# Optimization experiments

Measured on AMD Instinct MI355X. Metric: run time of the kernel, lower is better.

Reference implementation:

```python
import jax, jax.numpy as jnp
import numpy as np
from jax import lax

T, D, NH, CATS = 1024, 2048, 2048, 1000


def setup_inputs() -> dict:
    key = jax.random.key(0)
    ks = jax.random.split(key, 16)
    s = 0.02
    return {
        "x": jax.random.normal(ks[0], (T, D), dtype=jnp.float32),
        "Wh": jax.random.normal(ks[1], (NH, D), dtype=jnp.float32) * s,
        "Wz": jax.random.normal(ks[2], (NH, D), dtype=jnp.float32) * s,
        "Wr": jax.random.normal(ks[3], (NH, D), dtype=jnp.float32) * s,
        "Uh": jax.random.normal(ks[4], (NH, NH), dtype=jnp.float32) * s,
        "Uz": jax.random.normal(ks[5], (NH, NH), dtype=jnp.float32) * s,
        "bz": jax.random.normal(ks[6], (NH,), dtype=jnp.float32) * s,
        "Ur": jax.random.normal(ks[7], (NH, NH), dtype=jnp.float32) * s,
        "br": jax.random.normal(ks[8], (NH,), dtype=jnp.float32) * s,
        "Wout": jax.random.normal(ks[9], (CATS, NH), dtype=jnp.float32) * s,
        "h0": jax.random.normal(ks[10], (NH,), dtype=jnp.float32),
        "zt0": jax.random.normal(ks[11], (NH,), dtype=jnp.float32),
        "htilde0": jax.random.normal(ks[12], (NH,), dtype=jnp.float32),
        "hprev0": jax.random.normal(ks[13], (NH,), dtype=jnp.float32),
    }


def reference(x, Wh, Wz, Wr, Uh, Uz, bz, Ur, br, Wout, h0, zt0, htilde0, hprev0):
    # Batch the input projections over all timesteps: [T,d] @ [d,nh] -> [T,nh]
    xh = x @ Wh.T
    xz = x @ Wz.T
    xr = x @ Wr.T

    # Faithful to the original update ORDER: h is computed from the *stale*
    # zt/htilde (from the previous iteration), then gates are refreshed.
    # The original's hadamard(a, b) = linear(a, diag(b)) is exactly a * b.
    def step(carry, xs):
        h, zt, htilde, hprev = carry
        xh_t, xz_t, xr_t = xs
        h_new = (1.0 - zt) * hprev + zt * htilde
        zt_new = jax.nn.sigmoid(xz_t + hprev @ Uz.T + bz)
        htilde_new = jnp.tanh(xh_t + hprev @ Uh.T)
        # rt = sigmoid(xr_t + hprev @ Ur.T + br)  # computed in original, never used
        return (h_new, zt_new, htilde_new, h_new), None

    (h_fin, _, _, _), _ = lax.scan(step, (h0, zt0, htilde0, hprev0), (xh, xz, xr))
    logits = h_fin @ Wout.T  # [cats]
    return jax.nn.softmax(logits, axis=0)
```

## Files before the change

### kernel.cpp

```cpp
#include <hip/hip_runtime.h>
#include <math.h>

#define TT  1024
#define DD  2048
#define NHH 2048
#define CC  1000

#define SLOT_U64 4096

__global__ __launch_bounds__(256) void k_gemm(const float* __restrict__ X,
                                              const float* __restrict__ Wh,
                                              const float* __restrict__ Wz,
                                              const float* __restrict__ bz,
                                              float* __restrict__ XH,
                                              float* __restrict__ XZ) {
    __shared__ float As[32][68];
    __shared__ float Bs[32][68];
    const int z = blockIdx.z;
    const float* __restrict__ W = z ? Wz : Wh;
    float* __restrict__ OUT = z ? XZ : XH;
    const int n0 = blockIdx.x * 64;
    const int m0 = blockIdx.y * 64;
    const int tid = threadIdx.x;
    const int tx = tid & 15, ty = tid >> 4;
    const int lr = tid >> 2;
    const int lc = (tid & 3) * 8;

    float acc[4][4] = {};
    for (int k0 = 0; k0 < DD; k0 += 32) {
        float4 a0 = *(const float4*)&X[(size_t)(m0 + lr) * DD + k0 + lc];
        float4 a1 = *(const float4*)&X[(size_t)(m0 + lr) * DD + k0 + lc + 4];
        float4 b0 = *(const float4*)&W[(size_t)(n0 + lr) * DD + k0 + lc];
        float4 b1 = *(const float4*)&W[(size_t)(n0 + lr) * DD + k0 + lc + 4];
        As[lc+0][lr]=a0.x; As[lc+1][lr]=a0.y; As[lc+2][lr]=a0.z; As[lc+3][lr]=a0.w;
        As[lc+4][lr]=a1.x; As[lc+5][lr]=a1.y; As[lc+6][lr]=a1.z; As[lc+7][lr]=a1.w;
        Bs[lc+0][lr]=b0.x; Bs[lc+1][lr]=b0.y; Bs[lc+2][lr]=b0.z; Bs[lc+3][lr]=b0.w;
        Bs[lc+4][lr]=b1.x; Bs[lc+5][lr]=b1.y; Bs[lc+6][lr]=b1.z; Bs[lc+7][lr]=b1.w;
        __syncthreads();
#pragma unroll
        for (int kk = 0; kk < 32; ++kk) {
            float4 av = *(const float4*)&As[kk][ty * 4];
            float4 bv = *(const float4*)&Bs[kk][tx * 4];
            acc[0][0] = fmaf(av.x, bv.x, acc[0][0]); acc[0][1] = fmaf(av.x, bv.y, acc[0][1]);
            acc[0][2] = fmaf(av.x, bv.z, acc[0][2]); acc[0][3] = fmaf(av.x, bv.w, acc[0][3]);
            acc[1][0] = fmaf(av.y, bv.x, acc[1][0]); acc[1][1] = fmaf(av.y, bv.y, acc[1][1]);
            acc[1][2] = fmaf(av.y, bv.z, acc[1][2]); acc[1][3] = fmaf(av.y, bv.w, acc[1][3]);
            acc[2][0] = fmaf(av.z, bv.x, acc[2][0]); acc[2][1] = fmaf(av.z, bv.y, acc[2][1]);
            acc[2][2] = fmaf(av.z, bv.z, acc[2][2]); acc[2][3] = fmaf(av.z, bv.w, acc[2][3]);
            acc[3][0] = fmaf(av.w, bv.x, acc[3][0]); acc[3][1] = fmaf(av.w, bv.y, acc[3][1]);
            acc[3][2] = fmaf(av.w, bv.z, acc[3][2]); acc[3][3] = fmaf(av.w, bv.w, acc[3][3]);
        }
        __syncthreads();
    }
    float4 bias = make_float4(0.f, 0.f, 0.f, 0.f);
    if (z) bias = *(const float4*)&bz[n0 + tx * 4];
#pragma unroll
    for (int i = 0; i < 4; ++i) {
        float4 o = make_float4(acc[i][0] + bias.x, acc[i][1] + bias.y,
                               acc[i][2] + bias.z, acc[i][3] + bias.w);
        *(float4*)&OUT[(size_t)(m0 + ty * 4 + i) * NHH + n0 + tx * 4] = o;
    }
}

__global__ __launch_bounds__(256, 1) void k_recur(
    const float* __restrict__ XH, const float* __restrict__ XZ,
    const float* __restrict__ Uh, const float* __restrict__ Uz,
    const float* __restrict__ zt0, const float* __restrict__ ht0,
    const float* __restrict__ hp0,
    unsigned long long* __restrict__ Hbuf) {
    __shared__ float Hs[2][NHH];
    const int tid  = threadIdx.x;
    const int wave = tid >> 6, lane = tid & 63;
    const int wg   = blockIdx.x;
    const int base8 = wg * 8;
    const int e0 = base8 + 2 * wave;

    float u[4][32];
#pragma unroll
    for (int r = 0; r < 2; ++r) {
        const float* __restrict__ rowz = Uz + (size_t)(e0 + r) * NHH;
        const float* __restrict__ rowh = Uh + (size_t)(e0 + r) * NHH;
#pragma unroll
        for (int c = 0; c < 8; ++c) {
            float4 vz = *(const float4*)&rowz[c * 256 + lane * 4];
            float4 vh = *(const float4*)&rowh[c * 256 + lane * 4];
            u[r][c*4+0]=vz.x; u[r][c*4+1]=vz.y; u[r][c*4+2]=vz.z; u[r][c*4+3]=vz.w;
            u[2+r][c*4+0]=vh.x; u[2+r][c*4+1]=vh.y; u[2+r][c*4+2]=vh.z; u[2+r][c*4+3]=vh.w;
        }
    }

#pragma unroll
    for (int k = 0; k < 8; ++k) Hs[0][k * 256 + tid] = hp0[k * 256 + tid];

    float p_cur = 0.f;
    if (lane < 2) {
        const int e = e0 + lane;
        float z0 = zt0[e], g0 = ht0[e], p0 = hp0[e];
        p_cur = (1.0f - z0) * p0 + z0 * g0;
        __hip_atomic_store(&Hbuf[(size_t)1 * SLOT_U64 + wg * 16 + 2 * wave + lane],
            (1ull << 32) | (unsigned long long)__float_as_uint(p_cur),
            __ATOMIC_RELAXED, __HIP_MEMORY_SCOPE_AGENT);
    }
    float xz_n = 0.f, xh_n = 0.f;
    if (lane < 2) {
        xz_n = XZ[e0 + lane];
        xh_n = XH[e0 + lane];
    }
    __syncthreads();

    int p = 0;
    for (int t = 1; t < TT; ++t) {
        const unsigned long long* __restrict__ src = Hbuf + (size_t)(t & 3) * SLOT_U64;
        unsigned long long pv[8];
#pragma unroll
        for (int k = 0; k < 8; ++k) {
            const int e = k * 256 + tid;
            pv[k] = __hip_atomic_load(&src[(e >> 3) * 16 + (e & 7)],
                                      __ATOMIC_RELAXED, __HIP_MEMORY_SCOPE_AGENT);
        }
        const float xzv = xz_n, xhv = xh_n;
        if (lane < 2 && t < TT - 1) {
            xz_n = XZ[(size_t)t * NHH + e0 + lane];
            xh_n = XH[(size_t)t * NHH + e0 + lane];
        }

        float a0 = 0.f, a1 = 0.f, a2 = 0.f, a3 = 0.f;
#pragma unroll
        for (int c = 0; c < 8; ++c) {
            float4 h4 = *(const float4*)&Hs[p][c * 256 + lane * 4];
            a0 = fmaf(u[0][c*4+0], h4.x, fmaf(u[0][c*4+1], h4.y, fmaf(u[0][c*4+2], h4.z, fmaf(u[0][c*4+3], h4.w, a0))));
            a1 = fmaf(u[1][c*4+0], h4.x, fmaf(u[1][c*4+1], h4.y, fmaf(u[1][c*4+2], h4.z, fmaf(u[1][c*4+3], h4.w, a1))));
            a2 = fmaf(u[2][c*4+0], h4.x, fmaf(u[2][c*4+1], h4.y, fmaf(u[2][c*4+2], h4.z, fmaf(u[2][c*4+3], h4.w, a2))));
            a3 = fmaf(u[3][c*4+0], h4.x, fmaf(u[3][c*4+1], h4.y, fmaf(u[3][c*4+2], h4.z, fmaf(u[3][c*4+3], h4.w, a3))));
        }
#pragma unroll
        for (int off = 32; off > 0; off >>= 1) {
            a0 += __shfl_xor(a0, off); a1 += __shfl_xor(a1, off);
            a2 += __shfl_xor(a2, off); a3 += __shfl_xor(a3, off);
        }
        if (lane < 2) {
            float dz = lane ? a1 : a0;
            float dh = lane ? a3 : a2;
            float z = 1.0f / (1.0f + expf(-(xzv + dz)));
            float g = tanhf(xhv + dh);
            float pn = (1.0f - z) * p_cur + z * g;
            p_cur = pn;
            __hip_atomic_store(
                &Hbuf[(size_t)((t + 1) & 3) * SLOT_U64 + wg * 16 + 2 * wave + lane],
                ((unsigned long long)(unsigned)(t + 1) << 32)
                    | (unsigned long long)__float_as_uint(pn),
                __ATOMIC_RELAXED, __HIP_MEMORY_SCOPE_AGENT);
        }
        if (t == TT - 1) break;

        for (;;) {
            unsigned stale = 0;
#pragma unroll
            for (int k = 0; k < 8; ++k)
                if ((unsigned)(pv[k] >> 32) != (unsigned)t) stale |= (1u << k);
            if (!stale) break;
#pragma unroll
            for (int k = 0; k < 8; ++k)
                if (stale & (1u << k)) {
                    const int e = k * 256 + tid;
                    pv[k] = __hip_atomic_load(&src[(e >> 3) * 16 + (e & 7)],
                                              __ATOMIC_RELAXED, __HIP_MEMORY_SCOPE_AGENT);
                }
        }
#pragma unroll
        for (int k = 0; k < 8; ++k)
            Hs[p ^ 1][k * 256 + tid] = __uint_as_float((unsigned)pv[k]);
        __syncthreads();
        p ^= 1;
    }
}

__global__ __launch_bounds__(256) void k_logits(const unsigned long long* __restrict__ Hbuf,
                                                const float* __restrict__ Wout,
                                                float* __restrict__ lg) {
    __shared__ float Hs[NHH];
    const int tid = threadIdx.x;
    for (int k = tid; k < NHH; k += 256)
        Hs[k] = __uint_as_float((unsigned)Hbuf[(k >> 3) * 16 + (k & 7)]);
    __syncthreads();
    const int wave = tid >> 6, lane = tid & 63;
    const int row = blockIdx.x * 4 + wave;
    float a = 0.f;
#pragma unroll
    for (int c = 0; c < 8; ++c) {
        float4 w = *(const float4*)&Wout[(size_t)row * NHH + c * 256 + lane * 4];
        float4 h = *(const float4*)&Hs[c * 256 + lane * 4];
        a = fmaf(w.x, h.x, fmaf(w.y, h.y, fmaf(w.z, h.z, fmaf(w.w, h.w, a))));
    }
#pragma unroll
    for (int off = 32; off > 0; off >>= 1) a += __shfl_xor(a, off);
    if (lane == 0) lg[row] = a;
}

__global__ __launch_bounds__(1024) void k_softmax(const float* __restrict__ lg,
                                                  float* __restrict__ out) {
    const int i = threadIdx.x;
    __shared__ float red[16];
    __shared__ float bc[2];
    float v = (i < CC) ? lg[i] : -3.0e38f;
    float m = v;
#pragma unroll
    for (int off = 32; off > 0; off >>= 1) m = fmaxf(m, __shfl_xor(m, off));
    if ((i & 63) == 0) red[i >> 6] = m;
    __syncthreads();
    if (i == 0) { float mm = red[0]; for (int k = 1; k < 16; ++k) mm = fmaxf(mm, red[k]); bc[0] = mm; }
    __syncthreads();
    float e = (i < CC) ? expf(v - bc[0]) : 0.f;
    float s = e;
#pragma unroll
    for (int off = 32; off > 0; off >>= 1) s += __shfl_xor(s, off);
    if ((i & 63) == 0) red[i >> 6] = s;
    __syncthreads();
    if (i == 0) { float ss = 0.f; for (int k = 0; k < 16; ++k) ss += red[k]; bc[1] = ss; }
    __syncthreads();
    if (i < CC) out[i] = e / bc[1];
}

extern "C" void kernel_launch(void* const* d_in, const int* in_sizes, int n_in,
                              void* d_out, int out_size, void* d_ws, size_t ws_size,
                              hipStream_t stream) {
    const float* x    = (const float*)d_in[0];
    const float* Wh   = (const float*)d_in[1];
    const float* Wz   = (const float*)d_in[2];
    const float* Uh   = (const float*)d_in[4];
    const float* Uz   = (const float*)d_in[5];
    const float* bz   = (const float*)d_in[6];
    const float* Wout = (const float*)d_in[9];
    const float* zt0  = (const float*)d_in[11];
    const float* ht0  = (const float*)d_in[12];
    const float* hp0  = (const float*)d_in[13];
    float* out = (float*)d_out;

    float* XH = (float*)d_ws;
    float* XZ = XH + (size_t)TT * NHH;
    unsigned long long* Hbuf = (unsigned long long*)(XZ + (size_t)TT * NHH);
    float* lg = (float*)(Hbuf + 4 * SLOT_U64);

    k_gemm<<<dim3(NHH / 64, TT / 64, 2), dim3(256), 0, stream>>>(x, Wh, Wz, bz, XH, XZ);
    k_recur<<<dim3(256), dim3(256), 0, stream>>>(XH, XZ, Uh, Uz, zt0, ht0, hp0, Hbuf);
    k_logits<<<dim3(250), dim3(256), 0, stream>>>(Hbuf, Wout, lg);
    k_softmax<<<dim3(1), dim3(1024), 0, stream>>>(lg, out);
}
```

Baseline: 2.318 ms.

## Issue next-step hidden-state loads before spinning and compact the exchange buffer

The recurrence kernel now issues the atomic loads for the next timestep's hidden state right after publishing its own result, and only spins on staleness at the top of the following iteration. The aim is to overlap the cross-workgroup load latency with the loop tail. The first two steps are seeded locally from the initial values. The exchange buffer is packed densely (NHH slots instead of a padded 16-per-8 layout), which cuts memory footprint but may put more writers from different workgroups on the same cache lines.

```diff
diff --git a/kernel.cpp b/kernel.cpp
--- a/kernel.cpp
+++ b/kernel.cpp
@@ -5,8 +5,6 @@
 #define DD  2048
 #define NHH 2048
 #define CC  1000
-
-#define SLOT_U64 4096
 
 __global__ __launch_bounds__(256) void k_gemm(const float* __restrict__ X,
                                               const float* __restrict__ Wh,
@@ -71,8 +69,7 @@
     __shared__ float Hs[2][NHH];
     const int tid  = threadIdx.x;
     const int wave = tid >> 6, lane = tid & 63;
-    const int wg   = blockIdx.x;
-    const int base8 = wg * 8;
+    const int base8 = blockIdx.x * 8;
     const int e0 = base8 + 2 * wave;
 
     float u[4][32];
@@ -90,16 +87,16 @@
     }
 
 #pragma unroll
-    for (int k = 0; k < 8; ++k) Hs[0][k * 256 + tid] = hp0[k * 256 + tid];
-
+    for (int k = 0; k < 8; ++k) {
+        const int i = k * 256 + tid;
+        float p0 = hp0[i], z0 = zt0[i], g0 = ht0[i];
+        Hs[1][i] = p0;
+        Hs[0][i] = (1.0f - z0) * p0 + z0 * g0;
+    }
     float p_cur = 0.f;
     if (lane < 2) {
         const int e = e0 + lane;
-        float z0 = zt0[e], g0 = ht0[e], p0 = hp0[e];
-        p_cur = (1.0f - z0) * p0 + z0 * g0;
-        __hip_atomic_store(&Hbuf[(size_t)1 * SLOT_U64 + wg * 16 + 2 * wave + lane],
-            (1ull << 32) | (unsigned long long)__float_as_uint(p_cur),
-            __ATOMIC_RELAXED, __HIP_MEMORY_SCOPE_AGENT);
+        p_cur = (1.0f - zt0[e]) * hp0[e] + zt0[e] * ht0[e];
     }
     float xz_n = 0.f, xh_n = 0.f;
     if (lane < 2) {
@@ -108,26 +105,40 @@
     }
     __syncthreads();
 
-    int p = 0;
+    unsigned long long pv[8];
     for (int t = 1; t < TT; ++t) {
-        const unsigned long long* __restrict__ src = Hbuf + (size_t)(t & 3) * SLOT_U64;
-        unsigned long long pv[8];
-#pragma unroll
-        for (int k = 0; k < 8; ++k) {
-            const int e = k * 256 + tid;
-            pv[k] = __hip_atomic_load(&src[(e >> 3) * 16 + (e & 7)],
-                                      __ATOMIC_RELAXED, __HIP_MEMORY_SCOPE_AGENT);
-        }
+        if (t >= 3) {
+            const unsigned long long* __restrict__ src =
+                Hbuf + (size_t)((t - 1) & 3) * NHH;
+            for (;;) {
+                unsigned stale = 0;
+#pragma unroll
+                for (int k = 0; k < 8; ++k)
+                    if ((unsigned)(pv[k] >> 32) != (unsigned)(t - 1)) stale |= (1u << k);
+                if (!stale) break;
+#pragma unroll
+                for (int k = 0; k < 8; ++k)
+                    if (stale & (1u << k))
+                        pv[k] = __hip_atomic_load(&src[k * 256 + tid],
+                                                  __ATOMIC_RELAXED, __HIP_MEMORY_SCOPE_AGENT);
+            }
+#pragma unroll
+            for (int k = 0; k < 8; ++k)
+                Hs[t & 1][k * 256 + tid] = __uint_as_float((unsigned)pv[k]);
+            __syncthreads();
+        }
+
         const float xzv = xz_n, xhv = xh_n;
         if (lane < 2 && t < TT - 1) {
             xz_n = XZ[(size_t)t * NHH + e0 + lane];
             xh_n = XH[(size_t)t * NHH + e0 + lane];
         }
 
+        const float* __restrict__ H = Hs[t & 1];
         float a0 = 0.f, a1 = 0.f, a2 = 0.f, a3 = 0.f;
 #pragma unroll
         for (int c = 0; c < 8; ++c) {
-            float4 h4 = *(const float4*)&Hs[p][c * 256 + lane * 4];
+            float4 h4 = *(const float4*)&H[c * 256 + lane * 4];
             a0 = fmaf(u[0][c*4+0], h4.x, fmaf(u[0][c*4+1], h4.y, fmaf(u[0][c*4+2], h4.z, fmaf(u[0][c*4+3], h4.w, a0))));
             a1 = fmaf(u[1][c*4+0], h4.x, fmaf(u[1][c*4+1], h4.y, fmaf(u[1][c*4+2], h4.z, fmaf(u[1][c*4+3], h4.w, a1))));
             a2 = fmaf(u[2][c*4+0], h4.x, fmaf(u[2][c*4+1], h4.y, fmaf(u[2][c*4+2], h4.z, fmaf(u[2][c*4+3], h4.w, a2))));
@@ -138,6 +149,7 @@
             a0 += __shfl_xor(a0, off); a1 += __shfl_xor(a1, off);
             a2 += __shfl_xor(a2, off); a3 += __shfl_xor(a3, off);
         }
+
         if (lane < 2) {
             float dz = lane ? a1 : a0;
             float dh = lane ? a3 : a2;
@@ -145,33 +157,22 @@
             float g = tanhf(xhv + dh);
             float pn = (1.0f - z) * p_cur + z * g;
             p_cur = pn;
-            __hip_atomic_store(
-                &Hbuf[(size_t)((t + 1) & 3) * SLOT_U64 + wg * 16 + 2 * wave + lane],
+            __hip_atomic_store(&Hbuf[(size_t)((t + 1) & 3) * NHH + e0 + lane],
                 ((unsigned long long)(unsigned)(t + 1) << 32)
                     | (unsigned long long)__float_as_uint(pn),
                 __ATOMIC_RELAXED, __HIP_MEMORY_SCOPE_AGENT);
         }
         if (t == TT - 1) break;
 
-        for (;;) {
-            unsigned stale = 0;
+        if (t >= 2) {
+            const unsigned long long* __restrict__ s2 =
+                Hbuf + (size_t)(t & 3) * NHH;
 #pragma unroll
             for (int k = 0; k < 8; ++k)
-                if ((unsigned)(pv[k] >> 32) != (unsigned)t) stale |= (1u << k);
-            if (!stale) break;
-#pragma unroll
-            for (int k = 0; k < 8; ++k)
-                if (stale & (1u << k)) {
-                    const int e = k * 256 + tid;
-                    pv[k] = __hip_atomic_load(&src[(e >> 3) * 16 + (e & 7)],
-                                              __ATOMIC_RELAXED, __HIP_MEMORY_SCOPE_AGENT);
-                }
-        }
-#pragma unroll
-        for (int k = 0; k < 8; ++k)
-            Hs[p ^ 1][k * 256 + tid] = __uint_as_float((unsigned)pv[k]);
-        __syncthreads();
-        p ^= 1;
+                pv[k] = __hip_atomic_load(&s2[k * 256 + tid],
+                                          __ATOMIC_RELAXED, __HIP_MEMORY_SCOPE_AGENT);
+        }
+        if (t == 2) __syncthreads();
     }
 }
 
@@ -180,8 +181,7 @@
                                                 float* __restrict__ lg) {
     __shared__ float Hs[NHH];
     const int tid = threadIdx.x;
-    for (int k = tid; k < NHH; k += 256)
-        Hs[k] = __uint_as_float((unsigned)Hbuf[(k >> 3) * 16 + (k & 7)]);
+    for (int k = tid; k < NHH; k += 256) Hs[k] = __uint_as_float((unsigned)Hbuf[k]);
     __syncthreads();
     const int wave = tid >> 6, lane = tid & 63;
     const int row = blockIdx.x * 4 + wave;
@@ -239,7 +239,7 @@
     float* XH = (float*)d_ws;
     float* XZ = XH + (size_t)TT * NHH;
     unsigned long long* Hbuf = (unsigned long long*)(XZ + (size_t)TT * NHH);
-    float* lg = (float*)(Hbuf + 4 * SLOT_U64);
+    float* lg = (float*)(Hbuf + 4 * NHH);
 
     k_gemm<<<dim3(NHH / 64, TT / 64, 2), dim3(256), 0, stream>>>(x, Wh, Wz, bz, XH, XZ);
     k_recur<<<dim3(256), dim3(256), 0, stream>>>(XH, XZ, Uh, Uz, zt0, ht0, hp0, Hbuf);
```

New measurement: 2.543 ms. +9.7%, slower.
